# Kernel optimization log

Hardware: AMD Instinct MI355X
Metric: run time of the kernel (lower is better)

Reference implementation:

```python
import jax, jax.numpy as jnp
import numpy as np

N = 50000          # nodes
E = 1600000        # edges (before self-loops)
DIN = 128
HEADS = (8, 8, 4)
FEATS = (16, 16, 16)
NEG_SLOPE = 0.2


def setup_inputs() -> dict:
    key = jax.random.key(0)
    ks = jax.random.split(key, 2 + 4 * 3)
    inp = {
        "X": jax.random.normal(ks[0], (N, DIN), dtype=jnp.float32),
        "A": jax.random.randint(ks[1], (2, E), 0, N, dtype=jnp.int32),
    }
    in_dims = [DIN, HEADS[0] * FEATS[0], HEADS[1] * FEATS[1]]
    k = 2
    for i, (h, f) in enumerate(zip(HEADS, FEATS)):
        din = in_dims[i]
        concat = i + 1 < len(HEADS)
        inp[f"W{i+1}"] = jax.random.normal(ks[k], (din, h * f), dtype=jnp.float32) / np.float32(np.sqrt(din)); k += 1
        inp[f"as{i+1}"] = jax.random.normal(ks[k], (h, f), dtype=jnp.float32) * 0.1; k += 1
        inp[f"ad{i+1}"] = jax.random.normal(ks[k], (h, f), dtype=jnp.float32) * 0.1; k += 1
        inp[f"b{i+1}"] = jnp.zeros((h * f if concat else f,), dtype=jnp.float32); k += 1
    return inp


def _gat_conv(x, src, dst, W, a_src, a_dst, b, concat):
    # PyG-style GATConv (eval mode, self-loops already in src/dst)
    H, F = a_src.shape
    h = (x @ W).reshape(-1, H, F)                     # [N, H, F]
    e = jax.nn.leaky_relu((h * a_src).sum(-1)[src] + (h * a_dst).sum(-1)[dst], NEG_SLOPE)  # [Etot, H]
    m = jax.ops.segment_max(e, dst, num_segments=N)   # segment softmax over dst neighborhoods
    ex = jnp.exp(e - m[dst])
    s = jax.ops.segment_sum(ex, dst, num_segments=N)
    alpha = ex / (s[dst] + 1e-16)                     # [Etot, H]
    out = jax.ops.segment_sum(h[src] * alpha[:, :, None], dst, num_segments=N)  # [N, H, F]
    out = out.reshape(N, H * F) if concat else out.mean(axis=1)
    return out + b


def reference(X, A, W1, as1, ad1, b1, W2, as2, ad2, b2, W3, as3, ad3, b3):
    loops = jnp.arange(N, dtype=A.dtype)              # GATConv default add_self_loops=True
    src = jnp.concatenate([A[0], loops])
    dst = jnp.concatenate([A[1], loops])
    x = jax.nn.relu(_gat_conv(X, src, dst, W1, as1, ad1, b1, True))
    x = jax.nn.relu(_gat_conv(x, src, dst, W2, as2, ad2, b2, True))
    return _gat_conv(x, src, dst, W3, as3, ad3, b3, False)
```

## Files before the change

### kernel.cpp

```cpp
#include <hip/hip_runtime.h>
#include <hip/hip_bf16.h>

#define NN 50000
#define EE 1600000
#define DIN 128

#define BKT_SHIFT 6
#define NB ((NN + 63) >> 6)
#define BSLACK 2688
#define CHUNK 4096

typedef _Float16 half_t;
typedef __attribute__((ext_vector_type(2))) _Float16 half2_t;
typedef __attribute__((ext_vector_type(4))) _Float16 half4_t;
typedef __attribute__((ext_vector_type(8))) _Float16 half8_t;

__global__ void zero_gc(int* __restrict__ gcursor) {
    int i = blockIdx.x * 256 + threadIdx.x;
    if (i < NB) gcursor[i] = 0;
}

__global__ __launch_bounds__(256) void bin_kernel(const int* __restrict__ A,
                                                  int* __restrict__ gcursor,
                                                  int* __restrict__ binned, int e, int n) {
    __shared__ int lcount[NB];
    __shared__ int lbase[NB];
    int chunk0 = blockIdx.x * CHUNK;
    int cend = chunk0 + CHUNK;
    if (cend > e + n) cend = e + n;
    for (int i = threadIdx.x; i < NB; i += 256) lcount[i] = 0;
    __syncthreads();
    int sreg[16], dreg[16];
#pragma unroll
    for (int l = 0; l < 16; ++l) {
        int i = chunk0 + l * 256 + threadIdx.x;
        if (i < cend) {
            if (i < e) { sreg[l] = A[i]; dreg[l] = A[e + i]; }
            else       { sreg[l] = dreg[l] = i - e; }
            atomicAdd(&lcount[dreg[l] >> BKT_SHIFT], 1);
        } else {
            dreg[l] = -1;
        }
    }
    __syncthreads();
    for (int b = threadIdx.x; b < NB; b += 256) {
        int c = lcount[b];
        lbase[b] = c ? atomicAdd(&gcursor[b], c) : 0;
        lcount[b] = 0;
    }
    __syncthreads();
#pragma unroll
    for (int l = 0; l < 16; ++l) {
        if (dreg[l] >= 0) {
            int bkt = dreg[l] >> BKT_SHIFT;
            int pos = lbase[bkt] + atomicAdd(&lcount[bkt], 1);
            if (pos < BSLACK)
                binned[(size_t)bkt * BSLACK + pos] = (sreg[l] << 6) | (dreg[l] & 63);
        }
    }
}

__global__ __launch_bounds__(256) void fine_scatter(const int* __restrict__ binned,
                                                    const int* __restrict__ gcursor,
                                                    int* __restrict__ begE,
                                                    int* __restrict__ endE,
                                                    int* __restrict__ csr) {
    __shared__ int lc[64];
    __shared__ int scur[64];
    int b = blockIdx.x;
    int node0 = b << BKT_SHIFT;
    int cnt = gcursor[b];
    if (cnt > BSLACK) cnt = BSLACK;
    const int* bp = binned + (size_t)b * BSLACK;
    if (threadIdx.x < 64) lc[threadIdx.x] = 0;
    __syncthreads();
    for (int j = threadIdx.x; j < cnt; j += 256) atomicAdd(&lc[bp[j] & 63], 1);
    __syncthreads();
    if (threadIdx.x < 64) {
        int lane = threadIdx.x;
        int c = lc[lane];
        int v = c;
#pragma unroll
        for (int off = 1; off < 64; off <<= 1) {
            int u = __shfl_up(v, off, 64);
            if (lane >= off) v += u;
        }
        int begin = b * BSLACK + v - c;
        scur[lane] = begin;
        int node = node0 + lane;
        if (node < NN) {
            begE[node] = begin;
            endE[node] = begin + c;
        }
    }
    __syncthreads();
    for (int j = threadIdx.x; j < cnt; j += 256) {
        int v = bp[j];
        int pos = atomicAdd(&scur[v & 63], 1);
        csr[pos] = v >> 6;
    }
}

__global__ __launch_bounds__(256) void gemm_fused128(const float* __restrict__ A,
                                                     const float* __restrict__ B,
                                                     const float* __restrict__ asrc,
                                                     const float* __restrict__ adst,
                                                     half_t* __restrict__ C16,
                                                     float* __restrict__ ss,
                                                     float* __restrict__ ds, int M) {
    __shared__ float As[32][65];
    __shared__ float Bs[32][128];
    int tid = threadIdx.x;
    int tcol = tid & 15, trow = tid >> 4;
    int row0 = blockIdx.x * 64;
    float acc[4][8] = {};

    for (int k0 = 0; k0 < 128; k0 += 32) {
#pragma unroll
        for (int l = 0; l < 2; ++l) {
            int id = tid + l * 256;
            int r = id >> 3, c4 = (id & 7) * 4;
            int grow = row0 + r;
            float4 v = make_float4(0.f, 0.f, 0.f, 0.f);
            if (grow < M) v = *(const float4*)(A + (size_t)grow * 128 + k0 + c4);
            As[c4 + 0][r] = v.x;
            As[c4 + 1][r] = v.y;
            As[c4 + 2][r] = v.z;
            As[c4 + 3][r] = v.w;
        }
#pragma unroll
        for (int l = 0; l < 4; ++l) {
            int id = tid + l * 256;
            int r = id >> 5, c4 = (id & 31) * 4;
            *(float4*)(&Bs[r][c4]) = *(const float4*)(B + (size_t)(k0 + r) * 128 + c4);
        }
        __syncthreads();
#pragma unroll
        for (int k = 0; k < 32; ++k) {
            float a[4], b[8];
#pragma unroll
            for (int i = 0; i < 4; ++i) a[i] = As[k][trow * 4 + i];
#pragma unroll
            for (int j = 0; j < 8; ++j) b[j] = Bs[k][tcol * 8 + j];
#pragma unroll
            for (int i = 0; i < 4; ++i)
#pragma unroll
                for (int j = 0; j < 8; ++j) acc[i][j] += a[i] * b[j];
        }
        __syncthreads();
    }
    int hh = tcol >> 1;
    int fw0 = (tcol & 1) * 8;
#pragma unroll
    for (int i = 0; i < 4; ++i) {
        int grow = row0 + trow * 4 + i;
        float sp = 0.f, dp = 0.f;
#pragma unroll
        for (int j = 0; j < 8; ++j) {
            sp += acc[i][j] * asrc[hh * 16 + fw0 + j];
            dp += acc[i][j] * adst[hh * 16 + fw0 + j];
        }
        sp += __shfl_xor(sp, 1, 64);
        dp += __shfl_xor(dp, 1, 64);
        if (grow < M) {
            half8_t hv;
#pragma unroll
            for (int j = 0; j < 8; ++j) hv[j] = (half_t)acc[i][j];
            *(half8_t*)(C16 + (size_t)grow * 128 + tcol * 8) = hv;
            if ((tcol & 1) == 0) {
                ss[(size_t)grow * 8 + hh] = sp;
                ds[(size_t)grow * 8 + hh] = dp;
            }
        }
    }
}

__global__ __launch_bounds__(256) void gemm_fused64(const float* __restrict__ A,
                                                    const float* __restrict__ B,
                                                    const float* __restrict__ asrc,
                                                    const float* __restrict__ adst,
                                                    half_t* __restrict__ C16,
                                                    float* __restrict__ ss,
                                                    float* __restrict__ ds, int M) {
    __shared__ float As[32][65];
    __shared__ float Bs[32][64];
    int tid = threadIdx.x;
    int tx = tid & 15, ty = tid >> 4;
    int row0 = blockIdx.x * 64;
    float acc[4][4] = {};

    for (int k0 = 0; k0 < 128; k0 += 32) {
#pragma unroll
        for (int l = 0; l < 2; ++l) {
            int id = tid + l * 256;
            int r = id >> 3, c4 = (id & 7) * 4;
            int grow = row0 + r;
            float4 v = make_float4(0.f, 0.f, 0.f, 0.f);
            if (grow < M) v = *(const float4*)(A + (size_t)grow * 128 + k0 + c4);
            As[c4 + 0][r] = v.x;
            As[c4 + 1][r] = v.y;
            As[c4 + 2][r] = v.z;
            As[c4 + 3][r] = v.w;
        }
#pragma unroll
        for (int l = 0; l < 2; ++l) {
            int id = tid + l * 256;
            int r = id >> 4, c4 = (id & 15) * 4;
            *(float4*)(&Bs[r][c4]) = *(const float4*)(B + (size_t)(k0 + r) * 64 + c4);
        }
        __syncthreads();
#pragma unroll
        for (int k = 0; k < 32; ++k) {
            float a[4], b[4];
#pragma unroll
            for (int i = 0; i < 4; ++i) a[i] = As[k][ty * 4 + i];
#pragma unroll
            for (int j = 0; j < 4; ++j) b[j] = Bs[k][tx * 4 + j];
#pragma unroll
            for (int i = 0; i < 4; ++i)
#pragma unroll
                for (int j = 0; j < 4; ++j) acc[i][j] += a[i] * b[j];
        }
        __syncthreads();
    }
    int hh = tx >> 2;
    int fq = (tx & 3) * 4;
#pragma unroll
    for (int i = 0; i < 4; ++i) {
        int grow = row0 + ty * 4 + i;
        float sp = 0.f, dp = 0.f;
#pragma unroll
        for (int j = 0; j < 4; ++j) {
            sp += acc[i][j] * asrc[hh * 16 + fq + j];
            dp += acc[i][j] * adst[hh * 16 + fq + j];
        }
        sp += __shfl_xor(sp, 1, 64); sp += __shfl_xor(sp, 2, 64);
        dp += __shfl_xor(dp, 1, 64); dp += __shfl_xor(dp, 2, 64);
        if (grow < M) {
            half4_t hv;
#pragma unroll
            for (int j = 0; j < 4; ++j) hv[j] = (half_t)acc[i][j];
            *(half4_t*)(C16 + (size_t)grow * 64 + tx * 4) = hv;
            if ((tx & 3) == 0) {
                ss[(size_t)grow * 4 + hh] = sp;
                ds[(size_t)grow * 4 + hh] = dp;
            }
        }
    }
}

template <int H, int F, bool MEAN, bool RELU>
__global__ __launch_bounds__(256) void aggregate_qw(
    const half_t* __restrict__ h, const float* __restrict__ ss, const float* __restrict__ dsc_arr,
    const int* __restrict__ csr, const int* __restrict__ begE, const int* __restrict__ endE,
    const float* __restrict__ bias, float* __restrict__ out, int n) {
    constexpr int HF = H * F;
    constexpr int FPL = HF / 16;
    int wave = blockIdx.x * (blockDim.x >> 6) + (threadIdx.x >> 6);
    int lane = threadIdx.x & 63;
    if (wave >= n) return;
    int q = lane >> 4, ql = lane & 15;
    int hf = ql * FPL;
    int hh = hf / F;
    float dsc = dsc_arr[wave * H + hh];
    int begin = begE[wave], end = endE[wave];

    float ssum = 0.f;
    float acc[FPL];
#pragma unroll
    for (int k = 0; k < FPL; ++k) acc[k] = 0.f;

    int j = begin + q;
    for (; j + 4 < end; j += 8) {
        int s0 = csr[j], s1 = csr[j + 4];
        float e0 = ss[s0 * H + hh], e1 = ss[s1 * H + hh];
        const half_t* p0 = h + (size_t)s0 * HF + hf;
        const half_t* p1 = h + (size_t)s1 * HF + hf;
        e0 += dsc; e0 = (e0 > 0.f) ? e0 : 0.2f * e0;
        e1 += dsc; e1 = (e1 > 0.f) ? e1 : 0.2f * e1;
        float x0 = __expf(e0), x1 = __expf(e1);
        ssum += x0 + x1;
        if constexpr (FPL == 8) {
            half8_t t0 = *(const half8_t*)p0, t1 = *(const half8_t*)p1;
#pragma unroll
            for (int k = 0; k < 8; ++k) {
                acc[k] = fmaf(x0, (float)t0[k], acc[k]);
                acc[k] = fmaf(x1, (float)t1[k], acc[k]);
            }
        } else {
            half4_t t0 = *(const half4_t*)p0, t1 = *(const half4_t*)p1;
#pragma unroll
            for (int k = 0; k < 4; ++k) {
                acc[k] = fmaf(x0, (float)t0[k], acc[k]);
                acc[k] = fmaf(x1, (float)t1[k], acc[k]);
            }
        }
    }
    for (; j < end; j += 4) {
        int s = csr[j];
        float e = ss[s * H + hh] + dsc;
        e = (e > 0.f) ? e : 0.2f * e;
        float x = __expf(e);
        ssum += x;
        const half_t* hp = h + (size_t)s * HF + hf;
        if constexpr (FPL == 8) {
            half8_t t = *(const half8_t*)hp;
#pragma unroll
            for (int k = 0; k < 8; ++k) acc[k] = fmaf(x, (float)t[k], acc[k]);
        } else {
            half4_t t = *(const half4_t*)hp;
#pragma unroll
            for (int k = 0; k < 4; ++k) acc[k] = fmaf(x, (float)t[k], acc[k]);
        }
    }

    ssum += __shfl_xor(ssum, 16, 64);
    ssum += __shfl_xor(ssum, 32, 64);
#pragma unroll
    for (int k = 0; k < FPL; ++k) {
        acc[k] += __shfl_xor(acc[k], 16, 64);
        acc[k] += __shfl_xor(acc[k], 32, 64);
    }

    float inv = 1.f / (ssum + 1e-16f);
    if constexpr (!MEAN) {
        if (lane < 32) {
            int k0 = (lane >> 4) * 4;
            int f = (lane & 15) * FPL + k0;
            float v0 = acc[k0 + 0] * inv + bias[f + 0];
            float v1 = acc[k0 + 1] * inv + bias[f + 1];
            float v2 = acc[k0 + 2] * inv + bias[f + 2];
            float v3 = acc[k0 + 3] * inv + bias[f + 3];
            if (RELU) {
                v0 = fmaxf(v0, 0.f); v1 = fmaxf(v1, 0.f);
                v2 = fmaxf(v2, 0.f); v3 = fmaxf(v3, 0.f);
            }
            *(float4*)(out + (size_t)wave * HF + f) = make_float4(v0, v1, v2, v3);
        }
    } else {
        float val[FPL];
#pragma unroll
        for (int k = 0; k < FPL; ++k) {
            val[k] = acc[k] * inv;
            val[k] += __shfl_xor(val[k], 4, 64);
            val[k] += __shfl_xor(val[k], 8, 64);
        }
        if (lane < 4) {
            float v0 = val[0] * 0.25f + bias[lane * 4 + 0];
            float v1 = val[1] * 0.25f + bias[lane * 4 + 1];
            float v2 = val[2] * 0.25f + bias[lane * 4 + 2];
            float v3 = val[3] * 0.25f + bias[lane * 4 + 3];
            *(float4*)(out + (size_t)wave * F + lane * 4) = make_float4(v0, v1, v2, v3);
        }
    }
}

extern "C" void kernel_launch(void* const* d_in, const int* in_sizes, int n_in,
                              void* d_out, int out_size, void* d_ws, size_t ws_size,
                              hipStream_t stream) {
    const float* X  = (const float*)d_in[0];
    const int*   A  = (const int*)d_in[1];
    const float* W1 = (const float*)d_in[2];
    const float* as1 = (const float*)d_in[3];
    const float* ad1 = (const float*)d_in[4];
    const float* b1  = (const float*)d_in[5];
    const float* W2 = (const float*)d_in[6];
    const float* as2 = (const float*)d_in[7];
    const float* ad2 = (const float*)d_in[8];
    const float* b2  = (const float*)d_in[9];
    const float* W3 = (const float*)d_in[10];
    const float* as3 = (const float*)d_in[11];
    const float* ad3 = (const float*)d_in[12];
    const float* b3  = (const float*)d_in[13];

    const int N = NN, E = EE;
    const int Etot = E + N;

    char* p = (char*)d_ws;
    auto take = [&](size_t bytes) {
        char* r = p;
        p += (bytes + 255) & ~(size_t)255;
        return (void*)r;
    };
    half_t* hbuf  = (half_t*)take((size_t)N * 128 * 2);
    float* xA     = (float*)take((size_t)N * 128 * 4);
    float* xB     = (float*)take((size_t)N * 128 * 4);
    float* ssb    = (float*)take((size_t)N * 8 * 4);
    float* dsb    = (float*)take((size_t)N * 8 * 4);
    int* begE     = (int*)take((size_t)N * 4);
    int* endE     = (int*)take((size_t)N * 4);
    int* gcursor  = (int*)take((size_t)NB * 4);
    int* csr      = (int*)take((size_t)NB * BSLACK * 4);
    int* binned   = (int*)xA;

    zero_gc<<<(NB + 255) / 256, 256, 0, stream>>>(gcursor);
    bin_kernel<<<(Etot + CHUNK - 1) / CHUNK, 256, 0, stream>>>(A, gcursor, binned, E, N);
    fine_scatter<<<NB, 256, 0, stream>>>(binned, gcursor, begE, endE, csr);

    const int gemmRows = (N + 63) / 64;
    const int aggBlocks = (N + 3) / 4;

    gemm_fused128<<<gemmRows, 256, 0, stream>>>(X, W1, as1, ad1, hbuf, ssb, dsb, N);
    aggregate_qw<8, 16, false, true>
        <<<aggBlocks, 256, 0, stream>>>(hbuf, ssb, dsb, csr, begE, endE, b1, xA, N);

    gemm_fused128<<<gemmRows, 256, 0, stream>>>(xA, W2, as2, ad2, hbuf, ssb, dsb, N);
    aggregate_qw<8, 16, false, true>
        <<<aggBlocks, 256, 0, stream>>>(hbuf, ssb, dsb, csr, begE, endE, b2, xB, N);

    gemm_fused64<<<gemmRows, 256, 0, stream>>>(xB, W3, as3, ad3, hbuf, ssb, dsb, N);
    aggregate_qw<4, 16, true, false>
        <<<aggBlocks, 256, 0, stream>>>(hbuf, ssb, dsb, csr, begE, endE, b3, (float*)d_out, N);
}
```

Baseline: 378.6 us.

## Use split-fp16 MFMA GEMMs and emit hi/lo fp16 activations from aggregation

```diff
diff --git a/kernel.cpp b/kernel.cpp
--- a/kernel.cpp
+++ b/kernel.cpp
@@ -14,10 +14,56 @@
 typedef __attribute__((ext_vector_type(2))) _Float16 half2_t;
 typedef __attribute__((ext_vector_type(4))) _Float16 half4_t;
 typedef __attribute__((ext_vector_type(8))) _Float16 half8_t;
-
-__global__ void zero_gc(int* __restrict__ gcursor) {
-    int i = blockIdx.x * 256 + threadIdx.x;
-    if (i < NB) gcursor[i] = 0;
+typedef __attribute__((ext_vector_type(4))) float float4_t;
+
+__global__ __launch_bounds__(256) void prep_kernel(
+    const float* __restrict__ X, const float* __restrict__ W1,
+    const float* __restrict__ W2, const float* __restrict__ W3,
+    half_t* __restrict__ Xh, half_t* __restrict__ Xl,
+    half_t* __restrict__ B1h, half_t* __restrict__ B1l,
+    half_t* __restrict__ B2h, half_t* __restrict__ B2l,
+    half_t* __restrict__ B3h, half_t* __restrict__ B3l,
+    int* __restrict__ gcursor) {
+    int b = blockIdx.x;
+    if (b < 6250) {
+        int i = b * 256 + threadIdx.x;
+        if (i * 4 < NN * DIN) {
+            float4 xv = *(const float4*)(X + (size_t)i * 4);
+            half4_t hh, ll;
+            hh[0] = (half_t)xv.x; ll[0] = (half_t)(xv.x - (float)hh[0]);
+            hh[1] = (half_t)xv.y; ll[1] = (half_t)(xv.y - (float)hh[1]);
+            hh[2] = (half_t)xv.z; ll[2] = (half_t)(xv.z - (float)hh[2]);
+            hh[3] = (half_t)xv.w; ll[3] = (half_t)(xv.w - (float)hh[3]);
+            *(half4_t*)(Xh + (size_t)i * 4) = hh;
+            *(half4_t*)(Xl + (size_t)i * 4) = ll;
+        }
+    } else if (b < 6250 + 160) {
+        int id = (b - 6250) * 256 + threadIdx.x;
+        if (id < 16384) {
+            int kk = id >> 7, nn = id & 127;
+            float v = W1[id];
+            half_t h = (half_t)v;
+            B1h[nn * 128 + kk] = h;
+            B1l[nn * 128 + kk] = (half_t)(v - (float)h);
+        } else if (id < 32768) {
+            int id2 = id - 16384;
+            int kk = id2 >> 7, nn = id2 & 127;
+            float v = W2[id2];
+            half_t h = (half_t)v;
+            B2h[nn * 128 + kk] = h;
+            B2l[nn * 128 + kk] = (half_t)(v - (float)h);
+        } else {
+            int id3 = id - 32768;
+            int kk = id3 >> 6, nn = id3 & 63;
+            float v = W3[id3];
+            half_t h = (half_t)v;
+            B3h[nn * 128 + kk] = h;
+            B3l[nn * 128 + kk] = (half_t)(v - (float)h);
+        }
+    } else {
+        int i = (b - 6410) * 256 + threadIdx.x;
+        if (i < NB) gcursor[i] = 0;
+    }
 }
 
 __global__ __launch_bounds__(256) void bin_kernel(const int* __restrict__ A,
@@ -101,151 +147,93 @@
     }
 }
 
-__global__ __launch_bounds__(256) void gemm_fused128(const float* __restrict__ A,
-                                                     const float* __restrict__ B,
-                                                     const float* __restrict__ asrc,
-                                                     const float* __restrict__ adst,
-                                                     half_t* __restrict__ C16,
-                                                     float* __restrict__ ss,
-                                                     float* __restrict__ ds, int M) {
-    __shared__ float As[32][65];
-    __shared__ float Bs[32][128];
+template <int NT>
+__global__ __launch_bounds__(256) void gemm_mfma(
+    const half_t* __restrict__ Ah, const half_t* __restrict__ Al,
+    const half_t* __restrict__ Bth, const half_t* __restrict__ Btl,
+    const float* __restrict__ asrc, const float* __restrict__ adst,
+    half_t* __restrict__ C16, float* __restrict__ ss, float* __restrict__ ds, int M) {
+    constexpr int NCOL = NT * 16;
+    __shared__ __align__(16) half_t cs[4][16][NCOL + 8];
     int tid = threadIdx.x;
-    int tcol = tid & 15, trow = tid >> 4;
-    int row0 = blockIdx.x * 64;
-    float acc[4][8] = {};
-
-    for (int k0 = 0; k0 < 128; k0 += 32) {
-#pragma unroll
-        for (int l = 0; l < 2; ++l) {
-            int id = tid + l * 256;
-            int r = id >> 3, c4 = (id & 7) * 4;
-            int grow = row0 + r;
-            float4 v = make_float4(0.f, 0.f, 0.f, 0.f);
-            if (grow < M) v = *(const float4*)(A + (size_t)grow * 128 + k0 + c4);
-            As[c4 + 0][r] = v.x;
-            As[c4 + 1][r] = v.y;
-            As[c4 + 2][r] = v.z;
-            As[c4 + 3][r] = v.w;
-        }
-#pragma unroll
-        for (int l = 0; l < 4; ++l) {
-            int id = tid + l * 256;
-            int r = id >> 5, c4 = (id & 31) * 4;
-            *(float4*)(&Bs[r][c4]) = *(const float4*)(B + (size_t)(k0 + r) * 128 + c4);
-        }
-        __syncthreads();
-#pragma unroll
-        for (int k = 0; k < 32; ++k) {
-            float a[4], b[8];
-#pragma unroll
-            for (int i = 0; i < 4; ++i) a[i] = As[k][trow * 4 + i];
-#pragma unroll
-            for (int j = 0; j < 8; ++j) b[j] = Bs[k][tcol * 8 + j];
-#pragma unroll
-            for (int i = 0; i < 4; ++i)
-#pragma unroll
-                for (int j = 0; j < 8; ++j) acc[i][j] += a[i] * b[j];
-        }
-        __syncthreads();
-    }
-    int hh = tcol >> 1;
-    int fw0 = (tcol & 1) * 8;
-#pragma unroll
-    for (int i = 0; i < 4; ++i) {
-        int grow = row0 + trow * 4 + i;
-        float sp = 0.f, dp = 0.f;
-#pragma unroll
-        for (int j = 0; j < 8; ++j) {
-            sp += acc[i][j] * asrc[hh * 16 + fw0 + j];
-            dp += acc[i][j] * adst[hh * 16 + fw0 + j];
-        }
-        sp += __shfl_xor(sp, 1, 64);
-        dp += __shfl_xor(dp, 1, 64);
-        if (grow < M) {
-            half8_t hv;
-#pragma unroll
-            for (int j = 0; j < 8; ++j) hv[j] = (half_t)acc[i][j];
-            *(half8_t*)(C16 + (size_t)grow * 128 + tcol * 8) = hv;
-            if ((tcol & 1) == 0) {
-                ss[(size_t)grow * 8 + hh] = sp;
-                ds[(size_t)grow * 8 + hh] = dp;
-            }
-        }
-    }
-}
-
-__global__ __launch_bounds__(256) void gemm_fused64(const float* __restrict__ A,
-                                                    const float* __restrict__ B,
-                                                    const float* __restrict__ asrc,
-                                                    const float* __restrict__ adst,
-                                                    half_t* __restrict__ C16,
-                                                    float* __restrict__ ss,
-                                                    float* __restrict__ ds, int M) {
-    __shared__ float As[32][65];
-    __shared__ float Bs[32][64];
-    int tid = threadIdx.x;
-    int tx = tid & 15, ty = tid >> 4;
-    int row0 = blockIdx.x * 64;
-    float acc[4][4] = {};
-
-    for (int k0 = 0; k0 < 128; k0 += 32) {
-#pragma unroll
-        for (int l = 0; l < 2; ++l) {
-            int id = tid + l * 256;
-            int r = id >> 3, c4 = (id & 7) * 4;
-            int grow = row0 + r;
-            float4 v = make_float4(0.f, 0.f, 0.f, 0.f);
-            if (grow < M) v = *(const float4*)(A + (size_t)grow * 128 + k0 + c4);
-            As[c4 + 0][r] = v.x;
-            As[c4 + 1][r] = v.y;
-            As[c4 + 2][r] = v.z;
-            As[c4 + 3][r] = v.w;
-        }
-#pragma unroll
-        for (int l = 0; l < 2; ++l) {
-            int id = tid + l * 256;
-            int r = id >> 4, c4 = (id & 15) * 4;
-            *(float4*)(&Bs[r][c4]) = *(const float4*)(B + (size_t)(k0 + r) * 64 + c4);
-        }
-        __syncthreads();
-#pragma unroll
-        for (int k = 0; k < 32; ++k) {
-            float a[4], b[4];
-#pragma unroll
-            for (int i = 0; i < 4; ++i) a[i] = As[k][ty * 4 + i];
-#pragma unroll
-            for (int j = 0; j < 4; ++j) b[j] = Bs[k][tx * 4 + j];
-#pragma unroll
-            for (int i = 0; i < 4; ++i)
-#pragma unroll
-                for (int j = 0; j < 4; ++j) acc[i][j] += a[i] * b[j];
-        }
-        __syncthreads();
-    }
-    int hh = tx >> 2;
-    int fq = (tx & 3) * 4;
-#pragma unroll
-    for (int i = 0; i < 4; ++i) {
-        int grow = row0 + ty * 4 + i;
-        float sp = 0.f, dp = 0.f;
-#pragma unroll
-        for (int j = 0; j < 4; ++j) {
-            sp += acc[i][j] * asrc[hh * 16 + fq + j];
-            dp += acc[i][j] * adst[hh * 16 + fq + j];
-        }
-        sp += __shfl_xor(sp, 1, 64); sp += __shfl_xor(sp, 2, 64);
-        dp += __shfl_xor(dp, 1, 64); dp += __shfl_xor(dp, 2, 64);
-        if (grow < M) {
-            half4_t hv;
-#pragma unroll
-            for (int j = 0; j < 4; ++j) hv[j] = (half_t)acc[i][j];
-            *(half4_t*)(C16 + (size_t)grow * 64 + tx * 4) = hv;
-            if ((tx & 3) == 0) {
-                ss[(size_t)grow * 4 + hh] = sp;
-                ds[(size_t)grow * 4 + hh] = dp;
-            }
-        }
+    int w = tid >> 6, lane = tid & 63;
+    int m = lane & 15, q = lane >> 4;
+    int row0 = blockIdx.x * 64 + w * 16;
+
+    int ar = row0 + m;
+    if (ar >= M) ar = M - 1;
+    const half_t* pa = Ah + (size_t)ar * 128 + q * 8;
+    const half_t* pl = Al + (size_t)ar * 128 + q * 8;
+    half8_t ahf[4], alf[4];
+#pragma unroll
+    for (int k0 = 0; k0 < 4; ++k0) {
+        ahf[k0] = *(const half8_t*)(pa + k0 * 32);
+        alf[k0] = *(const half8_t*)(pl + k0 * 32);
+    }
+
+    float4_t acc[NT];
+#pragma unroll
+    for (int nt = 0; nt < NT; ++nt) {
+        acc[nt][0] = 0.f; acc[nt][1] = 0.f; acc[nt][2] = 0.f; acc[nt][3] = 0.f;
+    }
+
+#pragma unroll
+    for (int nt = 0; nt < NT; ++nt) {
+        const half_t* pbh = Bth + (size_t)(nt * 16 + m) * 128 + q * 8;
+        const half_t* pbl = Btl + (size_t)(nt * 16 + m) * 128 + q * 8;
+        half8_t bh[4], bl[4];
+#pragma unroll
+        for (int k0 = 0; k0 < 4; ++k0) {
+            bh[k0] = *(const half8_t*)(pbh + k0 * 32);
+            bl[k0] = *(const half8_t*)(pbl + k0 * 32);
+        }
+#pragma unroll
+        for (int k0 = 0; k0 < 4; ++k0) {
+            acc[nt] = __builtin_amdgcn_mfma_f32_16x16x32_f16(ahf[k0], bh[k0], acc[nt], 0, 0, 0);
+            acc[nt] = __builtin_amdgcn_mfma_f32_16x16x32_f16(ahf[k0], bl[k0], acc[nt], 0, 0, 0);
+            acc[nt] = __builtin_amdgcn_mfma_f32_16x16x32_f16(alf[k0], bh[k0], acc[nt], 0, 0, 0);
+        }
+    }
+
+    float asv[NT], adv[NT];
+#pragma unroll
+    for (int nt = 0; nt < NT; ++nt) {
+        asv[nt] = asrc[nt * 16 + m];
+        adv[nt] = adst[nt * 16 + m];
+    }
+#pragma unroll
+    for (int nt = 0; nt < NT; ++nt) {
+#pragma unroll
+        for (int r = 0; r < 4; ++r) {
+            float sp = acc[nt][r] * asv[nt];
+            float dp = acc[nt][r] * adv[nt];
+            sp += __shfl_xor(sp, 1, 64); sp += __shfl_xor(sp, 2, 64);
+            sp += __shfl_xor(sp, 4, 64); sp += __shfl_xor(sp, 8, 64);
+            dp += __shfl_xor(dp, 1, 64); dp += __shfl_xor(dp, 2, 64);
+            dp += __shfl_xor(dp, 4, 64); dp += __shfl_xor(dp, 8, 64);
+            int grow = row0 + q * 4 + r;
+            if (m == 0 && grow < M) {
+                ss[(size_t)grow * NT + nt] = sp;
+                ds[(size_t)grow * NT + nt] = dp;
+            }
+        }
+    }
+
+#pragma unroll
+    for (int nt = 0; nt < NT; ++nt)
+#pragma unroll
+        for (int r = 0; r < 4; ++r)
+            cs[w][q * 4 + r][nt * 16 + m] = (half_t)acc[nt][r];
+    constexpr int LPR = NCOL / 8;
+    constexpr int RPP = 64 / LPR;
+    constexpr int NP = 16 / RPP;
+    int rid = lane / LPR, cid = lane % LPR;
+#pragma unroll
+    for (int p = 0; p < NP; ++p) {
+        int r = p * RPP + rid;
+        int grow = row0 + r;
+        half8_t v = *(const half8_t*)&cs[w][r][cid * 8];
+        if (grow < M) *(half8_t*)(C16 + (size_t)grow * NCOL + cid * 8) = v;
     }
 }
 
@@ -253,7 +241,8 @@
 __global__ __launch_bounds__(256) void aggregate_qw(
     const half_t* __restrict__ h, const float* __restrict__ ss, const float* __restrict__ dsc_arr,
     const int* __restrict__ csr, const int* __restrict__ begE, const int* __restrict__ endE,
-    const float* __restrict__ bias, float* __restrict__ out, int n) {
+    const float* __restrict__ bias, half_t* __restrict__ outh, half_t* __restrict__ outl,
+    float* __restrict__ out, int n) {
     constexpr int HF = H * F;
     constexpr int FPL = HF / 16;
     int wave = blockIdx.x * (blockDim.x >> 6) + (threadIdx.x >> 6);
@@ -271,6 +260,42 @@
     for (int k = 0; k < FPL; ++k) acc[k] = 0.f;
 
     int j = begin + q;
+    for (; j + 12 < end; j += 16) {
+        int s0 = csr[j], s1 = csr[j + 4], s2 = csr[j + 8], s3 = csr[j + 12];
+        float e0 = ss[s0 * H + hh], e1 = ss[s1 * H + hh];
+        float e2 = ss[s2 * H + hh], e3 = ss[s3 * H + hh];
+        const half_t* p0 = h + (size_t)s0 * HF + hf;
+        const half_t* p1 = h + (size_t)s1 * HF + hf;
+        const half_t* p2 = h + (size_t)s2 * HF + hf;
+        const half_t* p3 = h + (size_t)s3 * HF + hf;
+        e0 += dsc; e0 = (e0 > 0.f) ? e0 : 0.2f * e0;
+        e1 += dsc; e1 = (e1 > 0.f) ? e1 : 0.2f * e1;
+        e2 += dsc; e2 = (e2 > 0.f) ? e2 : 0.2f * e2;
+        e3 += dsc; e3 = (e3 > 0.f) ? e3 : 0.2f * e3;
+        float x0 = __expf(e0), x1 = __expf(e1), x2 = __expf(e2), x3 = __expf(e3);
+        ssum += (x0 + x1) + (x2 + x3);
+        if constexpr (FPL == 8) {
+            half8_t t0 = *(const half8_t*)p0, t1 = *(const half8_t*)p1;
+            half8_t t2 = *(const half8_t*)p2, t3 = *(const half8_t*)p3;
+#pragma unroll
+            for (int k = 0; k < 8; ++k) {
+                acc[k] = fmaf(x0, (float)t0[k], acc[k]);
+                acc[k] = fmaf(x1, (float)t1[k], acc[k]);
+                acc[k] = fmaf(x2, (float)t2[k], acc[k]);
+                acc[k] = fmaf(x3, (float)t3[k], acc[k]);
+            }
+        } else {
+            half4_t t0 = *(const half4_t*)p0, t1 = *(const half4_t*)p1;
+            half4_t t2 = *(const half4_t*)p2, t3 = *(const half4_t*)p3;
+#pragma unroll
+            for (int k = 0; k < 4; ++k) {
+                acc[k] = fmaf(x0, (float)t0[k], acc[k]);
+                acc[k] = fmaf(x1, (float)t1[k], acc[k]);
+                acc[k] = fmaf(x2, (float)t2[k], acc[k]);
+                acc[k] = fmaf(x3, (float)t3[k], acc[k]);
+            }
+        }
+    }
     for (; j + 4 < end; j += 8) {
         int s0 = csr[j], s1 = csr[j + 4];
         float e0 = ss[s0 * H + hh], e1 = ss[s1 * H + hh];
@@ -327,15 +352,20 @@
         if (lane < 32) {
             int k0 = (lane >> 4) * 4;
             int f = (lane & 15) * FPL + k0;
-            float v0 = acc[k0 + 0] * inv + bias[f + 0];
-            float v1 = acc[k0 + 1] * inv + bias[f + 1];
-            float v2 = acc[k0 + 2] * inv + bias[f + 2];
-            float v3 = acc[k0 + 3] * inv + bias[f + 3];
-            if (RELU) {
-                v0 = fmaxf(v0, 0.f); v1 = fmaxf(v1, 0.f);
-                v2 = fmaxf(v2, 0.f); v3 = fmaxf(v3, 0.f);
-            }
-            *(float4*)(out + (size_t)wave * HF + f) = make_float4(v0, v1, v2, v3);
+            float v[4];
+#pragma unroll
+            for (int i = 0; i < 4; ++i) {
+                v[i] = acc[k0 + i] * inv + bias[f + i];
+                if (RELU) v[i] = fmaxf(v[i], 0.f);
+            }
+            half4_t hh4, ll4;
+#pragma unroll
+            for (int i = 0; i < 4; ++i) {
+                hh4[i] = (half_t)v[i];
+                ll4[i] = (half_t)(v[i] - (float)hh4[i]);
+            }
+            *(half4_t*)(outh + (size_t)wave * HF + f) = hh4;
+            *(half4_t*)(outl + (size_t)wave * HF + f) = ll4;
         }
     } else {
         float val[FPL];
@@ -382,33 +412,43 @@
         p += (bytes + 255) & ~(size_t)255;
         return (void*)r;
     };
-    half_t* hbuf  = (half_t*)take((size_t)N * 128 * 2);
-    float* xA     = (float*)take((size_t)N * 128 * 4);
-    float* xB     = (float*)take((size_t)N * 128 * 4);
+    half_t* Xh    = (half_t*)take((size_t)N * 128 * 2);
+    half_t* Xl    = (half_t*)take((size_t)N * 128 * 2);
+    half_t* C16   = (half_t*)take((size_t)N * 128 * 2);
+    half_t* o1h   = (half_t*)take((size_t)N * 128 * 2);
+    half_t* o1l   = (half_t*)take((size_t)N * 128 * 2);
     float* ssb    = (float*)take((size_t)N * 8 * 4);
     float* dsb    = (float*)take((size_t)N * 8 * 4);
     int* begE     = (int*)take((size_t)N * 4);
     int* endE     = (int*)take((size_t)N * 4);
     int* gcursor  = (int*)take((size_t)NB * 4);
     int* csr      = (int*)take((size_t)NB * BSLACK * 4);
-    int* binned   = (int*)xA;
-
-    zero_gc<<<(NB + 255) / 256, 256, 0, stream>>>(gcursor);
+    half_t* B1h   = (half_t*)take(128 * 128 * 2);
+    half_t* B1l   = (half_t*)take(128 * 128 * 2);
+    half_t* B2h   = (half_t*)take(128 * 128 * 2);
+    half_t* B2l   = (half_t*)take(128 * 128 * 2);
+    half_t* B3h   = (half_t*)take(64 * 128 * 2);
+    half_t* B3l   = (half_t*)take(64 * 128 * 2);
+    int* binned   = (int*)o1h;
+
+    prep_kernel<<<6414, 256, 0, stream>>>(X, W1, W2, W3, Xh, Xl,
+                                          B1h, B1l, B2h, B2l, B3h, B3l, gcursor);
     bin_kernel<<<(Etot + CHUNK - 1) / CHUNK, 256, 0, stream>>>(A, gcursor, binned, E, N);
     fine_scatter<<<NB, 256, 0, stream>>>(binned, gcursor, begE, endE, csr);
 
     const int gemmRows = (N + 63) / 64;
     const int aggBlocks = (N + 3) / 4;
 
-    gemm_fused128<<<gemmRows, 256, 0, stream>>>(X, W1, as1, ad1, hbuf, ssb, dsb, N);
+    gemm_mfma<8><<<gemmRows, 256, 0, stream>>>(Xh, Xl, B1h, B1l, as1, ad1, C16, ssb, dsb, N);
     aggregate_qw<8, 16, false, true>
-        <<<aggBlocks, 256, 0, stream>>>(hbuf, ssb, dsb, csr, begE, endE, b1, xA, N);
-
-    gemm_fused128<<<gemmRows, 256, 0, stream>>>(xA, W2, as2, ad2, hbuf, ssb, dsb, N);
+        <<<aggBlocks, 256, 0, stream>>>(C16, ssb, dsb, csr, begE, endE, b1, o1h, o1l, nullptr, N);
+
+    gemm_mfma<8><<<gemmRows, 256, 0, stream>>>(o1h, o1l, B2h, B2l, as2, ad2, C16, ssb, dsb, N);
     aggregate_qw<8, 16, false, true>
-        <<<aggBlocks, 256, 0, stream>>>(hbuf, ssb, dsb, csr, begE, endE, b2, xB, N);
-
-    gemm_fused64<<<gemmRows, 256, 0, stream>>>(xB, W3, as3, ad3, hbuf, ssb, dsb, N);
+        <<<aggBlocks, 256, 0, stream>>>(C16, ssb, dsb, csr, begE, endE, b2, Xh, Xl, nullptr, N);
+
+    gemm_mfma<4><<<gemmRows, 256, 0, stream>>>(Xh, Xl, B3h, B3l, as3, ad3, C16, ssb, dsb, N);
     aggregate_qw<4, 16, true, false>
-        <<<aggBlocks, 256, 0, stream>>>(hbuf, ssb, dsb, csr, begE, endE, b3, (float*)d_out, N);
-}
+        <<<aggBlocks, 256, 0, stream>>>(C16, ssb, dsb, csr, begE, endE, b3, nullptr, nullptr,
+                                        (float*)d_out, N);
+}
```

Result: slower. 407.8 us (+7.7%).
